# Kernel optimization log

Measured on AMD Instinct MI355X. Metric: run time of the kernel, lower is better.

## Reference

```python
import jax, jax.numpy as jnp
import numpy as np

QB = 127.0  # 8-bit symmetric activation range (input_bits=8)
EPS = 1e-5


def _weight_quant_ternary(w):
    # weight_quant_new: s = 1/mean(|w|); round(w*s).clamp(-1,1)
    s = 1.0 / jnp.clip(jnp.mean(jnp.abs(w)), EPS, None)
    return jnp.clip(jnp.round(w * s), -1.0, 1.0)


def setup_inputs() -> dict:
    key = jax.random.key(0)
    kx, kw = jax.random.split(key)
    B, S, IN, OUT = 4, 2048, 4096, 4096
    x = jax.random.normal(kx, (B, S, IN), dtype=jnp.float32)
    w_raw = jax.random.normal(kw, (OUT, IN), dtype=jnp.float32)
    # Module stores pre-quantized (packed) ternary weights as a buffer.
    w = _weight_quant_ternary(w_raw)  # values in {-1, 0, 1}, shape [OUT, IN]
    scale = jnp.float32(1.0)
    return {"x": x, "w": w, "scale": scale}


def reference(x, w, scale):
    # BitNet-style forward: per-token absmax int8 activation quantization,
    # ternary-weight matmul, then dequantize and apply module scale.
    gamma = jnp.clip(jnp.max(jnp.abs(x), axis=-1, keepdims=True), EPS, None)  # [B,S,1]
    x_q = jnp.clip(jnp.round(x * (QB / gamma)), -QB, QB)  # int8-valued floats
    y = jnp.einsum('bsi,oi->bso', x_q, w)  # low-bit GEMM accumulate
    return y * (gamma / QB) * scale
```

## Files before the change

kernel.cpp:

```cpp
#include <hip/hip_runtime.h>
#include <hip/hip_bf16.h>
#include <stdint.h>

#define QB 127.0f
#define EPS_G 1e-5f
#define KD 4096
#define ND 4096
#define BM 256
#define BN 256
#define BKB 128
#define NT (KD / BKB)
#define NI (NT / 2)

typedef int v4i __attribute__((ext_vector_type(4)));

#define GLOAD16(gp, lp)                                                        \
  __builtin_amdgcn_global_load_lds(                                            \
      (const __attribute__((address_space(1))) void*)(gp),                     \
      (__attribute__((address_space(3))) void*)(lp), 16, 0, 0)

#define BAR  __builtin_amdgcn_s_barrier()
#define WVM4 asm volatile("s_waitcnt vmcnt(4)" ::: "memory")

__global__ __launch_bounds__(256) void quant_fused_kernel(
    const float* __restrict__ x, const float* __restrict__ w,
    signed char* __restrict__ xq, signed char* __restrict__ wq,
    float* __restrict__ gamma_out, int M) {
  const int b = blockIdx.x;
  const int t = threadIdx.x;
  if (b < M) {
    const float4* xr = (const float4*)(x + (size_t)b * KD);
    float4 v[4];
    float m = 0.f;
#pragma unroll
    for (int i = 0; i < 4; ++i) {
      v[i] = xr[t + i * 256];
      m = fmaxf(m, fmaxf(fmaxf(fabsf(v[i].x), fabsf(v[i].y)),
                         fmaxf(fabsf(v[i].z), fabsf(v[i].w))));
    }
#pragma unroll
    for (int o = 32; o > 0; o >>= 1) m = fmaxf(m, __shfl_xor(m, o));
    __shared__ float red[4];
    if ((t & 63) == 0) red[t >> 6] = m;
    __syncthreads();
    m = fmaxf(fmaxf(red[0], red[1]), fmaxf(red[2], red[3]));
    const float gamma = fmaxf(m, EPS_G);
    if (t == 0) gamma_out[b] = gamma;
    const float inv = QB / gamma;
    char4* xqr = (char4*)(xq + (size_t)b * KD);
#pragma unroll
    for (int i = 0; i < 4; ++i) {
      char4 q;
      q.x = (signed char)(int)fminf(fmaxf(rintf(v[i].x * inv), -QB), QB);
      q.y = (signed char)(int)fminf(fmaxf(rintf(v[i].y * inv), -QB), QB);
      q.z = (signed char)(int)fminf(fmaxf(rintf(v[i].z * inv), -QB), QB);
      q.w = (signed char)(int)fminf(fmaxf(rintf(v[i].w * inv), -QB), QB);
      xqr[t + i * 256] = q;
    }
  } else {
    const int row = b - M;
    const float4* wr_ = (const float4*)(w + (size_t)row * KD);
    char4* wqr = (char4*)(wq + (size_t)row * KD);
#pragma unroll
    for (int i = 0; i < 4; ++i) {
      const float4 v = wr_[t + i * 256];
      char4 q;
      q.x = (signed char)(int)v.x;
      q.y = (signed char)(int)v.y;
      q.z = (signed char)(int)v.z;
      q.w = (signed char)(int)v.w;
      wqr[t + i * 256] = q;
    }
  }
}

__global__ __launch_bounds__(512, 2) void gemm_i8_8ph_kernel(
    const signed char* __restrict__ A,
    const signed char* __restrict__ B,
    const float* __restrict__ gamma,
    const float* __restrict__ scale_p,
    float* __restrict__ C) {
  extern __shared__ signed char lds[];
  signed char* ldsA = lds;
  signed char* ldsB = lds + 65536;

  const int t = threadIdx.x;
  const int lane = t & 63;
  const int wave = t >> 6;
  const int wr = wave >> 2;
  const int wcol = wave & 3;
  const int lr = lane & 15;
  const int lc = (lane >> 4) << 4;
  const int swzm = (lr & 7) << 4;

  const int bid = blockIdx.x;
  const int swz = (bid & 7) * 64 + (bid >> 3);
  const int brow = (swz >> 4) * BM;
  const int bcol = (swz & 15) * BN;

  const int c0 = t, c1 = t + 512;
  const int r0 = c0 >> 3, r1 = c1 >> 3;
  const int g0 = ((c0 & 7) << 4) ^ ((r0 & 7) << 4);
  const int g1 = ((c1 & 7) << 4) ^ ((r1 & 7) << 4);
  const signed char* sA0 = A + (size_t)(brow + r0) * KD + g0;
  const signed char* sA1 = A + (size_t)(brow + r1) * KD + g1;
  const signed char* sB0 = B + (size_t)(bcol + r0) * KD + g0;
  const signed char* sB1 = B + (size_t)(bcol + r1) * KD + g1;

#define STAGE_A(d, h, kt)                                                      \
  do {                                                                         \
    GLOAD16(sA0 + (size_t)(h) * 128 * KD + (kt) * BKB,                         \
            ldsA + (d) * 32768 + (h) * 16384 + c0 * 16);                       \
    GLOAD16(sA1 + (size_t)(h) * 128 * KD + (kt) * BKB,                         \
            ldsA + (d) * 32768 + (h) * 16384 + c1 * 16);                       \
  } while (0)
#define STAGE_B(d, h, kt)                                                      \
  do {                                                                         \
    GLOAD16(sB0 + (size_t)(h) * 128 * KD + (kt) * BKB,                         \
            ldsB + (d) * 32768 + (h) * 16384 + c0 * 16);                       \
    GLOAD16(sB1 + (size_t)(h) * 128 * KD + (kt) * BKB,                         \
            ldsB + (d) * 32768 + (h) * 16384 + c1 * 16);                       \
  } while (0)

#define LDA_H(d, mh)                                                           \
  _Pragma("unroll") for (int m_ = 0; m_ < 4; ++m_)                             \
  _Pragma("unroll") for (int k_ = 0; k_ < 2; ++k_)                             \
    af[m_][k_] = *(const v4i*)(ldsA + (d) * 32768 +                            \
        (wr * 128 + (mh) * 64 + m_ * 16 + lr) * 128 + ((k_ * 64 + lc) ^ swzm))
#define LDB_P(d, nh)                                                           \
  _Pragma("unroll") for (int n_ = 0; n_ < 2; ++n_)                             \
  _Pragma("unroll") for (int k_ = 0; k_ < 2; ++k_)                             \
    bf[(nh) * 2 + n_][k_] = *(const v4i*)(ldsB + (d) * 32768 +                 \
        (wcol * 64 + (nh) * 32 + n_ * 16 + lr) * 128 + ((k_ * 64 + lc) ^ swzm))

#define MFMA_Q(mh, nh)                                                         \
  do {                                                                         \
    __builtin_amdgcn_s_setprio(1);                                             \
    _Pragma("unroll") for (int m_ = 0; m_ < 4; ++m_)                           \
    _Pragma("unroll") for (int n_ = 0; n_ < 2; ++n_)                           \
    _Pragma("unroll") for (int k_ = 0; k_ < 2; ++k_)                           \
      acc[(mh) * 4 + m_][(nh) * 2 + n_] = __builtin_amdgcn_mfma_i32_16x16x64_i8( \
          af[m_][k_], bf[(nh) * 2 + n_][k_], acc[(mh) * 4 + m_][(nh) * 2 + n_], \
          0, 0, 0);                                                            \
    __builtin_amdgcn_s_setprio(0);                                             \
  } while (0)

  v4i acc[8][4];
#pragma unroll
  for (int i = 0; i < 8; ++i)
#pragma unroll
    for (int j = 0; j < 4; ++j) acc[i][j] = (v4i){0, 0, 0, 0};
  v4i af[4][2], bf[4][2];

  STAGE_B(0, 0, 0); STAGE_B(0, 1, 0); STAGE_A(0, 0, 0); STAGE_A(0, 1, 0);
  STAGE_B(1, 0, 1); STAGE_B(1, 1, 1);
  WVM4;
  BAR;
  LDB_P(0, 0);

#pragma unroll 1
  for (int i = 0; i < NI; ++i) {
    const int kc1 = 2 * i + 1;
    const int kn2 = (2 * i + 2) & (NT - 1);
    const int kn3 = (2 * i + 3) & (NT - 1);

    LDA_H(0, 0); STAGE_A(1, 0, kc1);
    BAR; MFMA_Q(0, 0); BAR;

    LDB_P(0, 1); STAGE_A(1, 1, kc1);
    BAR; MFMA_Q(0, 1); BAR;

    LDA_H(0, 1); STAGE_B(0, 0, kn2);
    BAR; MFMA_Q(1, 0); BAR;

    STAGE_B(0, 1, kn2); WVM4;
    BAR; LDB_P(1, 0); MFMA_Q(1, 1); BAR;

    LDA_H(1, 0); STAGE_A(0, 0, kn2);
    BAR; MFMA_Q(0, 0); BAR;

    LDB_P(1, 1); STAGE_A(0, 1, kn2);
    BAR; MFMA_Q(0, 1); BAR;

    LDA_H(1, 1); STAGE_B(1, 0, kn3);
    BAR; MFMA_Q(1, 0); BAR;

    STAGE_B(1, 1, kn3); WVM4;
    BAR; LDB_P(0, 0); MFMA_Q(1, 1); BAR;
  }

  const float scl = *scale_p;
  const int ccol0 = bcol + wcol * 64 + lr;
  const int crow0 = brow + wr * 128 + (lane >> 4) * 4;
#pragma unroll
  for (int m_ = 0; m_ < 8; ++m_) {
#pragma unroll
    for (int j = 0; j < 4; ++j) {
      const int row = crow0 + m_ * 16 + j;
      const float g = gamma[row] / QB;
#pragma unroll
      for (int n_ = 0; n_ < 4; ++n_) {
        __builtin_nontemporal_store(((float)acc[m_][n_][j] * g) * scl,
                                    &C[(size_t)row * ND + ccol0 + n_ * 16]);
      }
    }
  }
#undef STAGE_A
#undef STAGE_B
#undef LDA_H
#undef LDB_P
#undef MFMA_Q
}

extern "C" void kernel_launch(void* const* d_in, const int* in_sizes, int n_in,
                              void* d_out, int out_size, void* d_ws, size_t ws_size,
                              hipStream_t stream) {
  const float* x = (const float*)d_in[0];
  const float* w = (const float*)d_in[1];
  const float* scale = (const float*)d_in[2];
  float* out = (float*)d_out;

  const int M = in_sizes[0] / KD;

  signed char* wq = (signed char*)d_ws;
  signed char* xq = wq + (size_t)ND * KD;
  float* gamma = (float*)(xq + (size_t)M * KD);

  quant_fused_kernel<<<M + ND, 256, 0, stream>>>(x, w, xq, wq, gamma, M);

  const int nwg = (M / BM) * (ND / BN);
  gemm_i8_8ph_kernel<<<nwg, 512, 131072, stream>>>(xq, wq, gamma, scale, out);
}
```

Measured before the change: 380.5 us.

## Replace 8-phase ping-pong GEMM schedule with simple double-buffered single-phase loop

Replaces the hand-interleaved 8-phase schedule in the int8 GEMM with a plain double-buffered K loop. The old schedule used many barriers and partial vmcnt waits; the new loop issues the next tile's global-to-LDS loads, runs all MFMAs for the current tile in two k-steps, then syncs once. This cuts barrier count and code complexity. In exchange it loses the fine-grained overlap of LDS reads with MFMA and holds more fragment registers live at once.

```diff
diff --git a/kernel.cpp b/kernel.cpp
--- a/kernel.cpp
+++ b/kernel.cpp
@@ -10,7 +10,6 @@
 #define BN 256
 #define BKB 128
 #define NT (KD / BKB)
-#define NI (NT / 2)
 
 typedef int v4i __attribute__((ext_vector_type(4)));
 
@@ -18,9 +17,6 @@
   __builtin_amdgcn_global_load_lds(                                            \
       (const __attribute__((address_space(1))) void*)(gp),                     \
       (__attribute__((address_space(3))) void*)(lp), 16, 0, 0)
-
-#define BAR  __builtin_amdgcn_s_barrier()
-#define WVM4 asm volatile("s_waitcnt vmcnt(4)" ::: "memory")
 
 __global__ __launch_bounds__(256) void quant_fused_kernel(
     const float* __restrict__ x, const float* __restrict__ w,
@@ -74,7 +70,7 @@
   }
 }
 
-__global__ __launch_bounds__(512, 2) void gemm_i8_8ph_kernel(
+__global__ __launch_bounds__(512, 2) void gemm_i8_1ph_kernel(
     const signed char* __restrict__ A,
     const signed char* __restrict__ B,
     const float* __restrict__ gamma,
@@ -122,71 +118,47 @@
             ldsB + (d) * 32768 + (h) * 16384 + c1 * 16);                       \
   } while (0)
 
-#define LDA_H(d, mh)                                                           \
-  _Pragma("unroll") for (int m_ = 0; m_ < 4; ++m_)                             \
-  _Pragma("unroll") for (int k_ = 0; k_ < 2; ++k_)                             \
-    af[m_][k_] = *(const v4i*)(ldsA + (d) * 32768 +                            \
-        (wr * 128 + (mh) * 64 + m_ * 16 + lr) * 128 + ((k_ * 64 + lc) ^ swzm))
-#define LDB_P(d, nh)                                                           \
-  _Pragma("unroll") for (int n_ = 0; n_ < 2; ++n_)                             \
-  _Pragma("unroll") for (int k_ = 0; k_ < 2; ++k_)                             \
-    bf[(nh) * 2 + n_][k_] = *(const v4i*)(ldsB + (d) * 32768 +                 \
-        (wcol * 64 + (nh) * 32 + n_ * 16 + lr) * 128 + ((k_ * 64 + lc) ^ swzm))
-
-#define MFMA_Q(mh, nh)                                                         \
-  do {                                                                         \
-    __builtin_amdgcn_s_setprio(1);                                             \
-    _Pragma("unroll") for (int m_ = 0; m_ < 4; ++m_)                           \
-    _Pragma("unroll") for (int n_ = 0; n_ < 2; ++n_)                           \
-    _Pragma("unroll") for (int k_ = 0; k_ < 2; ++k_)                           \
-      acc[(mh) * 4 + m_][(nh) * 2 + n_] = __builtin_amdgcn_mfma_i32_16x16x64_i8( \
-          af[m_][k_], bf[(nh) * 2 + n_][k_], acc[(mh) * 4 + m_][(nh) * 2 + n_], \
-          0, 0, 0);                                                            \
-    __builtin_amdgcn_s_setprio(0);                                             \
-  } while (0)
-
   v4i acc[8][4];
 #pragma unroll
   for (int i = 0; i < 8; ++i)
 #pragma unroll
     for (int j = 0; j < 4; ++j) acc[i][j] = (v4i){0, 0, 0, 0};
-  v4i af[4][2], bf[4][2];
-
-  STAGE_B(0, 0, 0); STAGE_B(0, 1, 0); STAGE_A(0, 0, 0); STAGE_A(0, 1, 0);
-  STAGE_B(1, 0, 1); STAGE_B(1, 1, 1);
-  WVM4;
-  BAR;
-  LDB_P(0, 0);
+
+  STAGE_A(0, 0, 0); STAGE_A(0, 1, 0);
+  STAGE_B(0, 0, 0); STAGE_B(0, 1, 0);
+  __syncthreads();
 
 #pragma unroll 1
-  for (int i = 0; i < NI; ++i) {
-    const int kc1 = 2 * i + 1;
-    const int kn2 = (2 * i + 2) & (NT - 1);
-    const int kn3 = (2 * i + 3) & (NT - 1);
-
-    LDA_H(0, 0); STAGE_A(1, 0, kc1);
-    BAR; MFMA_Q(0, 0); BAR;
-
-    LDB_P(0, 1); STAGE_A(1, 1, kc1);
-    BAR; MFMA_Q(0, 1); BAR;
-
-    LDA_H(0, 1); STAGE_B(0, 0, kn2);
-    BAR; MFMA_Q(1, 0); BAR;
-
-    STAGE_B(0, 1, kn2); WVM4;
-    BAR; LDB_P(1, 0); MFMA_Q(1, 1); BAR;
-
-    LDA_H(1, 0); STAGE_A(0, 0, kn2);
-    BAR; MFMA_Q(0, 0); BAR;
-
-    LDB_P(1, 1); STAGE_A(0, 1, kn2);
-    BAR; MFMA_Q(0, 1); BAR;
-
-    LDA_H(1, 1); STAGE_B(1, 0, kn3);
-    BAR; MFMA_Q(1, 0); BAR;
-
-    STAGE_B(1, 1, kn3); WVM4;
-    BAR; LDB_P(0, 0); MFMA_Q(1, 1); BAR;
+  for (int kt = 0; kt < NT; ++kt) {
+    const int tn = (kt + 1) & (NT - 1);
+    const int dn = (kt + 1) & 1;
+    const int dc = kt & 1;
+
+    STAGE_A(dn, 0, tn); STAGE_A(dn, 1, tn);
+    STAGE_B(dn, 0, tn); STAGE_B(dn, 1, tn);
+
+#pragma unroll
+    for (int ks = 0; ks < 2; ++ks) {
+      v4i af[8], bf[4];
+#pragma unroll
+      for (int m_ = 0; m_ < 8; ++m_)
+        af[m_] = *(const v4i*)(ldsA + dc * 32768 +
+            (wr * 128 + m_ * 16 + lr) * 128 + ((ks * 64 + lc) ^ swzm));
+#pragma unroll
+      for (int n_ = 0; n_ < 4; ++n_)
+        bf[n_] = *(const v4i*)(ldsB + dc * 32768 +
+            (wcol * 64 + n_ * 16 + lr) * 128 + ((ks * 64 + lc) ^ swzm));
+      __builtin_amdgcn_s_setprio(1);
+#pragma unroll
+      for (int m_ = 0; m_ < 8; ++m_)
+#pragma unroll
+        for (int n_ = 0; n_ < 4; ++n_)
+          acc[m_][n_] = __builtin_amdgcn_mfma_i32_16x16x64_i8(
+              af[m_], bf[n_], acc[m_][n_], 0, 0, 0);
+      __builtin_amdgcn_s_setprio(0);
+    }
+
+    __syncthreads();
   }
 
   const float scl = *scale_p;
@@ -207,9 +179,6 @@
   }
 #undef STAGE_A
 #undef STAGE_B
-#undef LDA_H
-#undef LDB_P
-#undef MFMA_Q
 }
 
 extern "C" void kernel_launch(void* const* d_in, const int* in_sizes, int n_in,
@@ -229,5 +198,5 @@
   quant_fused_kernel<<<M + ND, 256, 0, stream>>>(x, w, xq, wq, gamma, M);
 
   const int nwg = (M / BM) * (ND / BN);
-  gemm_i8_8ph_kernel<<<nwg, 512, 131072, stream>>>(xq, wq, gamma, scale, out);
+  gemm_i8_1ph_kernel<<<nwg, 512, 131072, stream>>>(xq, wq, gamma, scale, out);
 }
```

Result: no change. 379.4 us (-0.3%).
